# Kernel optimization log

Measured on AMD Instinct MI355X. Metric: run time of the kernel, lower is better.

## Reference

```python
import jax, jax.numpy as jnp
import numpy as np

NUM_BINS = 23
SIGMA_RATIO = 0.5
SMOOTH_NR = 1e-07
SMOOTH_DR = 1e-07

BIN_CENTERS = jnp.linspace(0.0, 1.0, NUM_BINS)  # [bins]
_sigma = jnp.mean(BIN_CENTERS[1:] - BIN_CENTERS[:-1]) * SIGMA_RATIO
PRETERM = 1.0 / (2.0 * _sigma ** 2)


def setup_inputs() -> dict:
    key = jax.random.key(0)
    k1, k2 = jax.random.split(key)
    shape = (4, 1, 96, 96, 96)
    pred = jax.random.uniform(k1, shape, dtype=jnp.float32)
    target = jax.random.uniform(k2, shape, dtype=jnp.float32)
    return {"pred": pred, "target": target}


def _parzen(img):
    # img: [B, ...] -> weight [B, N, bins], probability [B, 1, bins]
    img = jnp.clip(img, 0.0, 1.0)
    img = img.reshape(img.shape[0], -1, 1)  # [B, N, 1]
    weight = jnp.exp(-PRETERM * (img - BIN_CENTERS[None, None, :]) ** 2)  # [B, N, bins]
    weight = weight / jnp.sum(weight, axis=-1, keepdims=True)
    probability = jnp.mean(weight, axis=-2, keepdims=True)  # [B, 1, bins]
    return weight, probability


def reference(pred, target):
    wa, pa = _parzen(pred)    # wa: [B, N, bins]
    wb, pb = _parzen(target)
    n = wa.shape[1]
    # joint histogram: [B, bins, bins]
    pab = jnp.einsum('bni,bnj->bij', wa, wb) / n
    # marginal product: [B, bins, bins]
    papb = jnp.einsum('bki,bkj->bij', pa, pb)
    mi = jnp.sum(pab * jnp.log((pab + SMOOTH_NR) / (papb + SMOOTH_DR) + SMOOTH_DR), axis=(1, 2))
    return -jnp.mean(mi)
```

## Files before the change

kernel.cpp:

```cpp
#include <hip/hip_runtime.h>
#include <math.h>


#define NBINS   23
#define NCELLS  529
#define NBATCH  4
#define NVOX    884736
#define PBLK    432
#define RPB     16
#define RBLK    (PBLK / RPB)
#define RS      72
#define IMGB    (24 * RS * 2)
#define WREG    (2 * IMGB)
#define SMEMB   (4 * WREG + 2048)

typedef float    vf4  __attribute__((ext_vector_type(4)));
typedef _Float16 h8   __attribute__((ext_vector_type(8)));
typedef float    f16v __attribute__((ext_vector_type(16)));

#define G1 0.13533528f
#define G2 3.3546263e-4f
#define G3 1.5229979e-8f

__device__ __forceinline__ float window7(float x, int& i0, float* w)
{
    x = fminf(fmaxf(x, 0.0f), 1.0f);
    int ka = (int)floorf(fmaf(x, 22.0f, 0.5f));
    i0 = min(max(ka - 3, 0), 16);
    float v  = fmaf((float)(i0 + 3), -(1.0f / 22.0f), x);
    float W0 = __expf(-968.0f * v * v);
    float R  = __expf(88.0f * v);
    float Ri = __builtin_amdgcn_rcpf(R);
    float R2 = R * R,   R3 = R2 * R;
    float R2i = Ri * Ri, R3i = R2i * Ri;
    w[0] = W0 * (R3i * G3);
    w[1] = W0 * (R2i * G2);
    w[2] = W0 * (Ri  * G1);
    w[3] = W0;
    w[4] = W0 * (R   * G1);
    w[5] = W0 * (R2  * G2);
    w[6] = W0 * (R3  * G3);
    return ((w[0] + w[6]) + (w[1] + w[5])) + ((w[2] + w[4]) + w[3]);
}

__global__ __launch_bounds__(256, 5)
void mi_mfma(const float* __restrict__ pred,
             const float* __restrict__ targ,
             float* __restrict__ partial,
             double* __restrict__ pab64,
             int* __restrict__ cnt)
{
    __shared__ __align__(16) char smem[SMEMB];

    if (blockIdx.x == 0 && blockIdx.y == 0) {
        for (int c = threadIdx.x; c < NBATCH * NCELLS; c += 256)
            pab64[c] = 0.0;
        if (threadIdx.x < 5) cnt[threadIdx.x] = 0;
    }

    const int p    = blockIdx.x;
    const int b    = blockIdx.y;
    const int wv   = threadIdx.x >> 6;
    const int lane = threadIdx.x & 63;
    const int m    = lane & 31;
    const int h    = lane >> 5;

    char* wbase = smem + wv * WREG;
    _Float16* Aimg = (_Float16*)wbase;
    _Float16* Bimg = (_Float16*)(wbase + IMGB);

    const size_t base = (size_t)b * NVOX + (size_t)p * 2048 + (size_t)wv * 512
                      + (size_t)lane * 8;
    const vf4* __restrict__ px4 = (const vf4*)(pred + base);
    const vf4* __restrict__ py4 = (const vf4*)(targ + base);
    vf4 xa = px4[0], xb = px4[1], ya = py4[0], yb = py4[1];
    float xs[8] = {xa.x, xa.y, xa.z, xa.w, xb.x, xb.y, xb.z, xb.w};
    float ys[8] = {ya.x, ya.y, ya.z, ya.w, yb.x, yb.y, yb.z, yb.w};

    f16v acc = {};

    #pragma unroll
    for (int c = 0; c < 8; ++c) {
        vf4 z = {0.f, 0.f, 0.f, 0.f};
        #pragma unroll
        for (int it = 0; it < 6; ++it)
            *(vf4*)(wbase + (it * 64 + lane) * 16) = z;
        if (lane < 48)
            *(vf4*)(wbase + (384 + lane) * 16) = z;

        int ia, ja;
        float wa[7], wb[7];
        float sa = window7(xs[c], ia, wa);
        float sb = window7(ys[c], ja, wb);
        float inv = __builtin_amdgcn_rcpf(sa * sb);

        #pragma unroll
        for (int t = 0; t < 7; ++t) {
            Aimg[(ia + t) * RS + lane] = (_Float16)(wa[t] * inv);
            Bimg[(ja + t) * RS + lane] = (_Float16)wb[t];
        }

        #pragma unroll
        for (int s = 0; s < 4; ++s) {
            h8 Af = *(const h8*)(Aimg + m * RS + 16 * s + 8 * h);
            h8 Bf = *(const h8*)(Bimg + m * RS + 16 * s + 8 * h);
            acc = __builtin_amdgcn_mfma_f32_32x32x16_f16(Af, Bf, acc, 0, 0, 0);
        }
    }

    float* tile = (float*)wbase;
    #pragma unroll
    for (int r = 0; r < 16; ++r) {
        int row = (r & 3) + 8 * (r >> 2) + 4 * h;
        tile[row * 33 + m] = acc[r];
    }
    __syncthreads();
    for (int c = threadIdx.x; c < NCELLS; c += 256) {
        int i = c / NBINS, j = c % NBINS;
        float s = 0.0f;
        #pragma unroll
        for (int w = 0; w < 4; ++w)
            s += ((const float*)(smem + w * WREG))[i * 33 + j];
        partial[((size_t)(b * PBLK + p)) * NCELLS + c] = s;
    }
}

__global__ __launch_bounds__(256)
void mi_reduce_batch(const float* __restrict__ partial,
                     double* __restrict__ pab64,
                     int* __restrict__ cnt,
                     double* __restrict__ mi_s,
                     float* __restrict__ out)
{
    __shared__ double s_pab[NCELLS];
    __shared__ double s_pa[NBINS];
    __shared__ double s_pb[NBINS];
    __shared__ double s_red[4];
    __shared__ int s_last;

    const int g = blockIdx.x;
    const int b = blockIdx.y;
    const int t = threadIdx.x;
    const float* __restrict__ src =
        partial + ((size_t)b * PBLK + (size_t)g * RPB) * NCELLS;

    double a0 = 0.0, a1 = 0.0, a2 = 0.0;
    #pragma unroll
    for (int p = 0; p < RPB; ++p) {
        const float* __restrict__ row = src + (size_t)p * NCELLS;
        a0 += (double)row[t];
        a1 += (double)row[256 + t];
        if (t < NCELLS - 512) a2 += (double)row[512 + t];
    }
    atomicAdd(&pab64[b * NCELLS + t],       a0);
    atomicAdd(&pab64[b * NCELLS + 256 + t], a1);
    if (t < NCELLS - 512) atomicAdd(&pab64[b * NCELLS + 512 + t], a2);

    __syncthreads();
    if (t == 0) {
        __threadfence();
        s_last = (atomicAdd(&cnt[b], 1) == RBLK - 1);
    }
    __syncthreads();
    if (!s_last) return;

    for (int c = t; c < NCELLS; c += 256)
        s_pab[c] = __hip_atomic_load(&pab64[b * NCELLS + c],
                                     __ATOMIC_RELAXED,
                                     __HIP_MEMORY_SCOPE_AGENT)
                   * (1.0 / (double)NVOX);
    __syncthreads();
    if (t < NBINS) {
        double r = 0.0, cl = 0.0;
        for (int j = 0; j < NBINS; ++j) {
            r  += s_pab[t * NBINS + j];
            cl += s_pab[j * NBINS + t];
        }
        s_pa[t] = r; s_pb[t] = cl;
    }
    __syncthreads();
    double tt = 0.0;
    for (int c = t; c < NCELLS; c += 256) {
        double pv   = s_pab[c];
        double papb = s_pa[c / NBINS] * s_pb[c % NBINS];
        tt += pv * log((pv + 1e-7) / (papb + 1e-7) + 1e-7);
    }
    #pragma unroll
    for (int off = 32; off > 0; off >>= 1) tt += __shfl_down(tt, off, 64);
    if ((t & 63) == 0) s_red[t >> 6] = tt;
    __syncthreads();

    if (t == 0) {
        double mi_b = s_red[0] + s_red[1] + s_red[2] + s_red[3];
        __hip_atomic_store(&mi_s[b], mi_b, __ATOMIC_RELEASE,
                           __HIP_MEMORY_SCOPE_AGENT);
        __threadfence();
        if (atomicAdd(&cnt[4], 1) == NBATCH - 1) {
            double m0 = __hip_atomic_load(&mi_s[0], __ATOMIC_RELAXED,
                                          __HIP_MEMORY_SCOPE_AGENT);
            double m1 = __hip_atomic_load(&mi_s[1], __ATOMIC_RELAXED,
                                          __HIP_MEMORY_SCOPE_AGENT);
            double m2 = __hip_atomic_load(&mi_s[2], __ATOMIC_RELAXED,
                                          __HIP_MEMORY_SCOPE_AGENT);
            double m3 = __hip_atomic_load(&mi_s[3], __ATOMIC_RELAXED,
                                          __HIP_MEMORY_SCOPE_AGENT);
            out[0] = (float)(-((m0 + m1) + (m2 + m3)) * 0.25);
        }
    }
}

extern "C" void kernel_launch(void* const* d_in, const int* in_sizes, int n_in,
                              void* d_out, int out_size, void* d_ws, size_t ws_size,
                              hipStream_t stream)
{
    const float* pred = (const float*)d_in[0];
    const float* targ = (const float*)d_in[1];
    float* out = (float*)d_out;
    char* ws = (char*)d_ws;

    const size_t off_pab64 =
        ((size_t)NBATCH * PBLK * NCELLS * 4 + 255) & ~(size_t)255;
    const size_t off_cnt = off_pab64 + (size_t)NBATCH * NCELLS * sizeof(double);
    const size_t off_mi  = (off_cnt + 5 * sizeof(int) + 7) & ~(size_t)7;

    float*  partial = (float*)ws;
    double* pab64   = (double*)(ws + off_pab64);
    int*    cnt     = (int*)(ws + off_cnt);
    double* mi_s    = (double*)(ws + off_mi);

    mi_mfma<<<dim3(PBLK, NBATCH), 256, 0, stream>>>(pred, targ, partial,
                                                    pab64, cnt);
    mi_reduce_batch<<<dim3(RBLK, NBATCH), 256, 0, stream>>>(partial, pab64,
                                                            cnt, mi_s, out);
}
```

Baseline: 100.7 us.

## Compute dense 23-bin weights and pack two voxels per lane for MFMA

The 7-tap sliding window with per-voxel LDS zeroing and scattered 16-bit stores is replaced by full 23-bin Parzen weights for every voxel. Two voxels are packed per lane as half2 and written with ds_write2_b32, so each 32x32x16 MFMA chain covers a K of 128 and the shared-memory clears go away. The cost is much more exp and VALU work per voxel, far more registers for the weight arrays, and lower occupancy (launch bound cut from 5 to 3). Padding rows 23-31 of the operand tiles are read from adjacent shared memory and only feed discarded output rows.

```diff
diff --git a/kernel.cpp b/kernel.cpp
--- a/kernel.cpp
+++ b/kernel.cpp
@@ -9,12 +9,14 @@
 #define PBLK    432
 #define RPB     16
 #define RBLK    (PBLK / RPB)
-#define RS      72
-#define IMGB    (24 * RS * 2)
-#define WREG    (2 * IMGB)
-#define SMEMB   (4 * WREG + 2048)
-
-typedef float    vf4  __attribute__((ext_vector_type(4)));
+#define RSH     136
+#define RSB     272
+#define IMG4    (23 * RSB)
+#define WREG    (2 * IMG4)
+#define SMEMB   (4 * WREG + 2496)
+
+typedef float    vf2  __attribute__((ext_vector_type(2)));
+typedef _Float16 h2t  __attribute__((ext_vector_type(2)));
 typedef _Float16 h8   __attribute__((ext_vector_type(8)));
 typedef float    f16v __attribute__((ext_vector_type(16)));
 
@@ -22,28 +24,38 @@
 #define G2 3.3546263e-4f
 #define G3 1.5229979e-8f
 
-__device__ __forceinline__ float window7(float x, int& i0, float* w)
+#define DSW2(A, LO, HI, O0, O1)                                         \
+    asm volatile("ds_write2_b32 %0, %1, %2 offset0:" #O0 " offset1:" #O1 \
+                 :: "v"(A), "v"(LO), "v"(HI) : "memory")
+
+__device__ __forceinline__ float window23(float x, float* w)
 {
     x = fminf(fmaxf(x, 0.0f), 1.0f);
-    int ka = (int)floorf(fmaf(x, 22.0f, 0.5f));
-    i0 = min(max(ka - 3, 0), 16);
-    float v  = fmaf((float)(i0 + 3), -(1.0f / 22.0f), x);
-    float W0 = __expf(-968.0f * v * v);
-    float R  = __expf(88.0f * v);
-    float Ri = __builtin_amdgcn_rcpf(R);
-    float R2 = R * R,   R3 = R2 * R;
-    float R2i = Ri * Ri, R3i = R2i * Ri;
-    w[0] = W0 * (R3i * G3);
-    w[1] = W0 * (R2i * G2);
-    w[2] = W0 * (Ri  * G1);
-    w[3] = W0;
-    w[4] = W0 * (R   * G1);
-    w[5] = W0 * (R2  * G2);
-    w[6] = W0 * (R3  * G3);
-    return ((w[0] + w[6]) + (w[1] + w[5])) + ((w[2] + w[4]) + w[3]);
-}
-
-__global__ __launch_bounds__(256, 5)
+    #pragma unroll
+    for (int q = 0; q < 6; ++q) {
+        float vq = fmaf((float)(4 * q), -(1.0f / 22.0f), x);
+        float W0 = __expf(-968.0f * (vq * vq));
+        float R  = __expf(88.0f * vq);
+        float p  = W0;
+        w[4 * q] = p;
+        p *= R;  w[4 * q + 1] = p * G1;
+        p *= R;  w[4 * q + 2] = p * G2;
+        if (q < 5) { p *= R; w[4 * q + 3] = p * G3; }
+    }
+    float s0 = ((w[0] + w[1]) + (w[2] + w[3])) + ((w[4] + w[5]) + (w[6] + w[7]));
+    float s1 = ((w[8] + w[9]) + (w[10] + w[11]))
+             + ((w[12] + w[13]) + (w[14] + w[15]));
+    float s2 = ((w[16] + w[17]) + (w[18] + w[19])) + ((w[20] + w[21]) + w[22]);
+    return (s0 + s1) + s2;
+}
+
+__device__ __forceinline__ unsigned int pk(float a, float b)
+{
+    h2t t; t[0] = (_Float16)a; t[1] = (_Float16)b;
+    return __builtin_bit_cast(unsigned int, t);
+}
+
+__global__ __launch_bounds__(256, 3)
 void mi_mfma(const float* __restrict__ pred,
              const float* __restrict__ targ,
              float* __restrict__ partial,
@@ -66,44 +78,59 @@
     const int h    = lane >> 5;
 
     char* wbase = smem + wv * WREG;
-    _Float16* Aimg = (_Float16*)wbase;
-    _Float16* Bimg = (_Float16*)(wbase + IMGB);
-
-    const size_t base = (size_t)b * NVOX + (size_t)p * 2048 + (size_t)wv * 512
-                      + (size_t)lane * 8;
-    const vf4* __restrict__ px4 = (const vf4*)(pred + base);
-    const vf4* __restrict__ py4 = (const vf4*)(targ + base);
-    vf4 xa = px4[0], xb = px4[1], ya = py4[0], yb = py4[1];
-    float xs[8] = {xa.x, xa.y, xa.z, xa.w, xb.x, xb.y, xb.z, xb.w};
-    float ys[8] = {ya.x, ya.y, ya.z, ya.w, yb.x, yb.y, yb.z, yb.w};
+    const _Float16* AimgH = (const _Float16*)wbase;
+    const _Float16* BimgH = (const _Float16*)(wbase + IMG4);
+
+    const unsigned int awA = (unsigned int)(uintptr_t)wbase + 4u * lane;
+    const unsigned int awB = awA + IMG4;
+
+    const size_t base2 = (size_t)b * NVOX + (size_t)p * 2048
+                       + (size_t)wv * 512 + 2 * (size_t)lane;
 
     f16v acc = {};
 
-    #pragma unroll
-    for (int c = 0; c < 8; ++c) {
-        vf4 z = {0.f, 0.f, 0.f, 0.f};
-        #pragma unroll
-        for (int it = 0; it < 6; ++it)
-            *(vf4*)(wbase + (it * 64 + lane) * 16) = z;
-        if (lane < 48)
-            *(vf4*)(wbase + (384 + lane) * 16) = z;
-
-        int ia, ja;
-        float wa[7], wb[7];
-        float sa = window7(xs[c], ia, wa);
-        float sb = window7(ys[c], ja, wb);
-        float inv = __builtin_amdgcn_rcpf(sa * sb);
-
-        #pragma unroll
-        for (int t = 0; t < 7; ++t) {
-            Aimg[(ia + t) * RS + lane] = (_Float16)(wa[t] * inv);
-            Bimg[(ja + t) * RS + lane] = (_Float16)wb[t];
-        }
-
-        #pragma unroll
-        for (int s = 0; s < 4; ++s) {
-            h8 Af = *(const h8*)(Aimg + m * RS + 16 * s + 8 * h);
-            h8 Bf = *(const h8*)(Bimg + m * RS + 16 * s + 8 * h);
+    #pragma unroll 1
+    for (int c = 0; c < 4; ++c) {
+        vf2 xv = *(const vf2*)(pred + base2 + (size_t)c * 128);
+        vf2 yv = *(const vf2*)(targ + base2 + (size_t)c * 128);
+
+        float wx0[23], wx1[23], wy0[23], wy1[23];
+        float sx0 = window23(xv.x, wx0);
+        float sx1 = window23(xv.y, wx1);
+        float sy0 = window23(yv.x, wy0);
+        float sy1 = window23(yv.y, wy1);
+        float i0 = __builtin_amdgcn_rcpf(sx0 * sy0);
+        float i1 = __builtin_amdgcn_rcpf(sx1 * sy1);
+
+        unsigned int dA[23], dB[23];
+        #pragma unroll
+        for (int r = 0; r < 23; ++r) {
+            dA[r] = pk(wx0[r] * i0, wx1[r] * i1);
+            dB[r] = pk(wy0[r], wy1[r]);
+        }
+
+        #pragma unroll
+        for (int gg = 0; gg < 5; ++gg) {
+            unsigned int aA = awA + gg * 1088u, aB = awB + gg * 1088u;
+            DSW2(aA, dA[4 * gg],     dA[4 * gg + 1], 0, 68);
+            DSW2(aA, dA[4 * gg + 2], dA[4 * gg + 3], 136, 204);
+            DSW2(aB, dB[4 * gg],     dB[4 * gg + 1], 0, 68);
+            DSW2(aB, dB[4 * gg + 2], dB[4 * gg + 3], 136, 204);
+        }
+        {
+            unsigned int aA = awA + 5u * 1088u, aB = awB + 5u * 1088u;
+            DSW2(aA, dA[20], dA[21], 0, 68);
+            DSW2(aB, dB[20], dB[21], 0, 68);
+            asm volatile("ds_write_b32 %0, %1 offset:544"
+                         :: "v"(aA), "v"(dA[22]) : "memory");
+            asm volatile("ds_write_b32 %0, %1 offset:544"
+                         :: "v"(aB), "v"(dB[22]) : "memory");
+        }
+
+        #pragma unroll
+        for (int s = 0; s < 8; ++s) {
+            h8 Af = *(const h8*)(AimgH + m * RSH + 16 * s + 8 * h);
+            h8 Bf = *(const h8*)(BimgH + m * RSH + 16 * s + 8 * h);
             acc = __builtin_amdgcn_mfma_f32_32x32x16_f16(Af, Bf, acc, 0, 0, 0);
         }
     }
```

Measured after the change: 108.1 us. 7.3% more time.
